# Optimization experiments

Measured on AMD Instinct MI355X. Metric: run time of the kernel, lower is better.

Reference implementation:

```python
import jax, jax.numpy as jnp
import numpy as np

WIN_SIZE = 11
SIGMA = 1.5
DATA_RANGE = 1.0
K1, K2 = 0.01, 0.03


def _gaussian_1d(size=WIN_SIZE, sigma=SIGMA):
    coords = np.arange(size, dtype=np.float32) - (size - 1) / 2.0
    g = np.exp(-(coords ** 2) / (2.0 * sigma ** 2))
    g = g / g.sum()
    return jnp.asarray(g, dtype=jnp.float32)


def _gaussian_blur(x):
    # Separable depthwise Gaussian blur, VALID padding (matches pytorch-msssim).
    B, C, H, W = x.shape
    g = _gaussian_1d().astype(x.dtype)
    kh = jnp.tile(g.reshape(1, 1, WIN_SIZE, 1), (C, 1, 1, 1))
    kw = jnp.tile(g.reshape(1, 1, 1, WIN_SIZE), (C, 1, 1, 1))
    dn = ('NCHW', 'OIHW', 'NCHW')
    x = jax.lax.conv_general_dilated(x, kh, (1, 1), 'VALID',
                                     dimension_numbers=dn, feature_group_count=C)
    x = jax.lax.conv_general_dilated(x, kw, (1, 1), 'VALID',
                                     dimension_numbers=dn, feature_group_count=C)
    return x


def _ssim(X, Y):
    C1 = (K1 * DATA_RANGE) ** 2
    C2 = (K2 * DATA_RANGE) ** 2

    mu1 = _gaussian_blur(X)
    mu2 = _gaussian_blur(Y)
    mu1_sq = mu1 * mu1
    mu2_sq = mu2 * mu2
    mu1_mu2 = mu1 * mu2

    sigma1_sq = _gaussian_blur(X * X) - mu1_sq
    sigma2_sq = _gaussian_blur(Y * Y) - mu2_sq
    sigma12 = _gaussian_blur(X * Y) - mu1_mu2

    cs_map = (2.0 * sigma12 + C2) / (sigma1_sq + sigma2_sq + C2)
    ssim_map = ((2.0 * mu1_mu2 + C1) / (mu1_sq + mu2_sq + C1)) * cs_map

    ssim_per_channel = ssim_map.mean(axis=(2, 3))  # [B, C]
    return ssim_per_channel


def setup_inputs() -> dict:
    key = jax.random.key(0)
    k1, k2 = jax.random.split(key)
    predictions = jax.random.uniform(k1, (32, 3, 512, 512), dtype=jnp.float32)
    labels = jax.random.uniform(k2, (32, 3, 512, 512), dtype=jnp.float32)
    return {"predictions": predictions, "labels": labels}


def reference(predictions, labels):
    ssim_per_channel = _ssim(predictions, labels)
    # nonnegative_ssim=True -> relu; size_average=True -> scalar mean
    ssim_val = jax.nn.relu(ssim_per_channel).mean()
    return 1.0 - ssim_val
```

## Files before the change

kernel.cpp:

```cpp
#include <hip/hip_runtime.h>


#define IMG 512
#define OUT_DIM 502
#define WIN 11
#define BH 32
#define NPHASE (BH + WIN - 1)
#define NPLANES 96

#define GAUSS_INIT {0.00102838f, 0.00759875f, 0.03600077f, 0.10936071f, \
                    0.21300553f, 0.26601172f, 0.21300553f, 0.10936071f, \
                    0.03600077f, 0.00759875f, 0.00102838f}

template<int PH>
__device__ __forceinline__ void phase_step(
    int base, int r0, int c, int cbase,
    const float* __restrict__ Xp, const float* __restrict__ Yp,
    float w0, float w1, float w2, float w3, float w4, float w5,
    float w6, float w7, float w8, float w9, float w10, float w11,
    float (&a)[5][WIN], float& local) {
    constexpr float G[WIN] = GAUSS_INIT;
    const int p = base + PH;
    if (p >= NPHASE) return;
    const int rr = min(r0 + p, IMG - 1);
    const float* px = Xp + rr * IMG + cbase;
    const float* py = Yp + rr * IMG + cbase;

    float h0 = 0.f, h1 = 0.f, h2 = 0.f, h3 = 0.f, h4 = 0.f;
#define PAIR(i, ka, kb) do {                                      \
        const float2 xv = *(const float2*)(px + 2 * (i));         \
        const float2 yv = *(const float2*)(py + 2 * (i));         \
        h0 = fmaf(w##ka, xv.x, h0);                               \
        h1 = fmaf(w##ka, yv.x, h1);                               \
        h2 = fmaf(w##ka, xv.x * xv.x, h2);                        \
        h3 = fmaf(w##ka, yv.x * yv.x, h3);                        \
        h4 = fmaf(w##ka, xv.x * yv.x, h4);                        \
        h0 = fmaf(w##kb, xv.y, h0);                               \
        h1 = fmaf(w##kb, yv.y, h1);                               \
        h2 = fmaf(w##kb, xv.y * xv.y, h2);                        \
        h3 = fmaf(w##kb, yv.y * yv.y, h3);                        \
        h4 = fmaf(w##kb, xv.y * yv.y, h4);                        \
    } while (0)
    PAIR(0, 0, 1); PAIR(1, 2, 3); PAIR(2, 4, 5);
    PAIR(3, 6, 7); PAIR(4, 8, 9); PAIR(5, 10, 11);
#undef PAIR

#define ACC(d) do {                                               \
        constexpr int s = (PH - (d) + 2 * WIN) % WIN;             \
        constexpr float g = G[(d)];                               \
        if ((d) == 0) {                                           \
            a[0][s] = g * h0; a[1][s] = g * h1; a[2][s] = g * h2; \
            a[3][s] = g * h3; a[4][s] = g * h4;                   \
        } else {                                                  \
            a[0][s] = fmaf(g, h0, a[0][s]);                       \
            a[1][s] = fmaf(g, h1, a[1][s]);                       \
            a[2][s] = fmaf(g, h2, a[2][s]);                       \
            a[3][s] = fmaf(g, h3, a[3][s]);                       \
            a[4][s] = fmaf(g, h4, a[4][s]);                       \
        }                                                         \
    } while (0)
    ACC(0); ACC(1); ACC(2); ACC(3); ACC(4); ACC(5);
    ACC(6); ACC(7); ACC(8); ACC(9); ACC(10);
#undef ACC

    if (p >= WIN - 1) {
        const int o = r0 + p - (WIN - 1);
        if (o < OUT_DIM && c < OUT_DIM) {
            constexpr int se = (PH + 1) % WIN;
            const float C1 = 0.0001f, C2 = 0.0009f;
            const float m1 = a[0][se], m2 = a[1][se];
            const float m1sq = m1 * m1, m2sq = m2 * m2, m12 = m1 * m2;
            const float s1  = a[2][se] - m1sq;
            const float s2  = a[3][se] - m2sq;
            const float s12 = a[4][se] - m12;
            const float num = (2.f * m12 + C1) * (2.f * s12 + C2);
            const float den = (m1sq + m2sq + C1) * (s1 + s2 + C2);
            local += num * __builtin_amdgcn_rcpf(den);
        }
    }
}

__global__ __launch_bounds__(256)
__attribute__((amdgpu_waves_per_eu(2, 4)))
void ssim_stream(const float* __restrict__ X,
                 const float* __restrict__ Y,
                 float* __restrict__ planeSums) {
    constexpr float G[WIN] = GAUSS_INIT;
    const int tid = threadIdx.x;
    const int r0 = blockIdx.x * BH;
    const int c = (blockIdx.y << 8) + tid;
    const int plane = blockIdx.z;
    const size_t pbase = (size_t)plane * IMG * IMG;
    const float* Xp = X + pbase;
    const float* Yp = Y + pbase;
    const int cbase = min(c & ~1, IMG - 12);

    const bool odd = (c & 1) != 0;
    const float w0  = odd ? 0.f   : G[0];
    const float w1  = odd ? G[0]  : G[1];
    const float w2  = odd ? G[1]  : G[2];
    const float w3  = odd ? G[2]  : G[3];
    const float w4  = odd ? G[3]  : G[4];
    const float w5  = odd ? G[4]  : G[5];
    const float w6  = odd ? G[5]  : G[6];
    const float w7  = odd ? G[6]  : G[7];
    const float w8  = odd ? G[7]  : G[8];
    const float w9  = odd ? G[8]  : G[9];
    const float w10 = odd ? G[9]  : G[10];
    const float w11 = odd ? G[10] : 0.f;

    float a[5][WIN];
    float local = 0.f;

    for (int base = 0; base < 44; base += WIN) {
        phase_step<0>(base, r0, c, cbase, Xp, Yp, w0,w1,w2,w3,w4,w5,w6,w7,w8,w9,w10,w11, a, local);
        phase_step<1>(base, r0, c, cbase, Xp, Yp, w0,w1,w2,w3,w4,w5,w6,w7,w8,w9,w10,w11, a, local);
        phase_step<2>(base, r0, c, cbase, Xp, Yp, w0,w1,w2,w3,w4,w5,w6,w7,w8,w9,w10,w11, a, local);
        phase_step<3>(base, r0, c, cbase, Xp, Yp, w0,w1,w2,w3,w4,w5,w6,w7,w8,w9,w10,w11, a, local);
        phase_step<4>(base, r0, c, cbase, Xp, Yp, w0,w1,w2,w3,w4,w5,w6,w7,w8,w9,w10,w11, a, local);
        phase_step<5>(base, r0, c, cbase, Xp, Yp, w0,w1,w2,w3,w4,w5,w6,w7,w8,w9,w10,w11, a, local);
        phase_step<6>(base, r0, c, cbase, Xp, Yp, w0,w1,w2,w3,w4,w5,w6,w7,w8,w9,w10,w11, a, local);
        phase_step<7>(base, r0, c, cbase, Xp, Yp, w0,w1,w2,w3,w4,w5,w6,w7,w8,w9,w10,w11, a, local);
        phase_step<8>(base, r0, c, cbase, Xp, Yp, w0,w1,w2,w3,w4,w5,w6,w7,w8,w9,w10,w11, a, local);
        phase_step<9>(base, r0, c, cbase, Xp, Yp, w0,w1,w2,w3,w4,w5,w6,w7,w8,w9,w10,w11, a, local);
        phase_step<10>(base, r0, c, cbase, Xp, Yp, w0,w1,w2,w3,w4,w5,w6,w7,w8,w9,w10,w11, a, local);
    }

    #pragma unroll
    for (int off = 32; off > 0; off >>= 1)
        local += __shfl_down(local, off, 64);
    __shared__ float red[4];
    if ((tid & 63) == 0) red[tid >> 6] = local;
    __syncthreads();
    if (tid == 0)
        atomicAdd(&planeSums[plane], (red[0] + red[1]) + (red[2] + red[3]));
}

__global__ __launch_bounds__(128) void ssim_finalize(const float* __restrict__ planeSums,
                                                     float* __restrict__ out) {
    const int tid = threadIdx.x;
    float v = 0.f;
    if (tid < NPLANES) {
        const float m = planeSums[tid] * (1.0f / (float)(OUT_DIM * OUT_DIM));
        v = fmaxf(m, 0.f);
    }
    #pragma unroll
    for (int off = 32; off > 0; off >>= 1)
        v += __shfl_down(v, off, 64);
    __shared__ float red[2];
    if ((tid & 63) == 0) red[tid >> 6] = v;
    __syncthreads();
    if (tid == 0) out[0] = 1.0f - (red[0] + red[1]) * (1.0f / (float)NPLANES);
}

extern "C" void kernel_launch(void* const* d_in, const int* in_sizes, int n_in,
                              void* d_out, int out_size, void* d_ws, size_t ws_size,
                              hipStream_t stream) {
    const float* X = (const float*)d_in[0];
    const float* Y = (const float*)d_in[1];
    float* out = (float*)d_out;
    float* ws  = (float*)d_ws;

    hipMemsetAsync(ws, 0, NPLANES * sizeof(float), stream);

    dim3 grid((OUT_DIM + BH - 1) / BH, 2, NPLANES);
    ssim_stream<<<grid, 256, 0, stream>>>(X, Y, ws);
    ssim_finalize<<<1, 128, 0, stream>>>(ws, out);
}
```

Baseline: 331.8 us.

## Compute two adjacent output columns per thread to share loads and products

Each thread now produces two adjacent output columns instead of one. The x*x, y*y and x*y products and the row loads are computed once and feed both horizontal filters, replacing the per-thread odd/even weight selection. The grid's column dimension is removed, so the launch uses half as many threads. In exchange, each thread carries twice as many vertical accumulators (110 floats), which raises register pressure and may lower occupancy or cause spills.

```diff
diff --git a/kernel.cpp b/kernel.cpp
--- a/kernel.cpp
+++ b/kernel.cpp
@@ -14,49 +14,70 @@
 
 template<int PH>
 __device__ __forceinline__ void phase_step(
-    int base, int r0, int c, int cbase,
+    int base, int r0row, int c0, int cbase,
     const float* __restrict__ Xp, const float* __restrict__ Yp,
-    float w0, float w1, float w2, float w3, float w4, float w5,
-    float w6, float w7, float w8, float w9, float w10, float w11,
-    float (&a)[5][WIN], float& local) {
+    float (&a)[5][2][WIN], float& local) {
     constexpr float G[WIN] = GAUSS_INIT;
     const int p = base + PH;
     if (p >= NPHASE) return;
-    const int rr = min(r0 + p, IMG - 1);
+    const int rr = min(r0row + p, IMG - 1);
     const float* px = Xp + rr * IMG + cbase;
     const float* py = Yp + rr * IMG + cbase;
 
-    float h0 = 0.f, h1 = 0.f, h2 = 0.f, h3 = 0.f, h4 = 0.f;
-#define PAIR(i, ka, kb) do {                                      \
+    float h0a = 0.f, h1a = 0.f, h2a = 0.f, h3a = 0.f, h4a = 0.f;
+    float h0b = 0.f, h1b = 0.f, h2b = 0.f, h3b = 0.f, h4b = 0.f;
+#define ELT(j, xe, ye) do {                                       \
+        const float xx = (xe) * (xe);                             \
+        const float yy = (ye) * (ye);                             \
+        const float xy = (xe) * (ye);                             \
+        if ((j) <= 10) {                                          \
+            const float ga = G[(j) <= 10 ? (j) : 0];              \
+            h0a = fmaf(ga, (xe), h0a);                            \
+            h1a = fmaf(ga, (ye), h1a);                            \
+            h2a = fmaf(ga, xx, h2a);                              \
+            h3a = fmaf(ga, yy, h3a);                              \
+            h4a = fmaf(ga, xy, h4a);                              \
+        }                                                         \
+        if ((j) >= 1) {                                           \
+            const float gb = G[(j) >= 1 ? (j) - 1 : 0];           \
+            h0b = fmaf(gb, (xe), h0b);                            \
+            h1b = fmaf(gb, (ye), h1b);                            \
+            h2b = fmaf(gb, xx, h2b);                              \
+            h3b = fmaf(gb, yy, h3b);                              \
+            h4b = fmaf(gb, xy, h4b);                              \
+        }                                                         \
+    } while (0)
+#define PAIR(i) do {                                              \
         const float2 xv = *(const float2*)(px + 2 * (i));         \
         const float2 yv = *(const float2*)(py + 2 * (i));         \
-        h0 = fmaf(w##ka, xv.x, h0);                               \
-        h1 = fmaf(w##ka, yv.x, h1);                               \
-        h2 = fmaf(w##ka, xv.x * xv.x, h2);                        \
-        h3 = fmaf(w##ka, yv.x * yv.x, h3);                        \
-        h4 = fmaf(w##ka, xv.x * yv.x, h4);                        \
-        h0 = fmaf(w##kb, xv.y, h0);                               \
-        h1 = fmaf(w##kb, yv.y, h1);                               \
-        h2 = fmaf(w##kb, xv.y * xv.y, h2);                        \
-        h3 = fmaf(w##kb, yv.y * yv.y, h3);                        \
-        h4 = fmaf(w##kb, xv.y * yv.y, h4);                        \
+        ELT(2 * (i),     xv.x, yv.x);                             \
+        ELT(2 * (i) + 1, xv.y, yv.y);                             \
     } while (0)
-    PAIR(0, 0, 1); PAIR(1, 2, 3); PAIR(2, 4, 5);
-    PAIR(3, 6, 7); PAIR(4, 8, 9); PAIR(5, 10, 11);
+    PAIR(0); PAIR(1); PAIR(2); PAIR(3); PAIR(4); PAIR(5);
 #undef PAIR
+#undef ELT
 
 #define ACC(d) do {                                               \
-        constexpr int s = (PH - (d) + 2 * WIN) % WIN;             \
-        constexpr float g = G[(d)];                               \
+        const int s = (PH - (d) + 2 * WIN) % WIN;                 \
+        const float g = G[(d)];                                   \
         if ((d) == 0) {                                           \
-            a[0][s] = g * h0; a[1][s] = g * h1; a[2][s] = g * h2; \
-            a[3][s] = g * h3; a[4][s] = g * h4;                   \
+            a[0][0][s] = g * h0a; a[1][0][s] = g * h1a;           \
+            a[2][0][s] = g * h2a; a[3][0][s] = g * h3a;           \
+            a[4][0][s] = g * h4a;                                 \
+            a[0][1][s] = g * h0b; a[1][1][s] = g * h1b;           \
+            a[2][1][s] = g * h2b; a[3][1][s] = g * h3b;           \
+            a[4][1][s] = g * h4b;                                 \
         } else {                                                  \
-            a[0][s] = fmaf(g, h0, a[0][s]);                       \
-            a[1][s] = fmaf(g, h1, a[1][s]);                       \
-            a[2][s] = fmaf(g, h2, a[2][s]);                       \
-            a[3][s] = fmaf(g, h3, a[3][s]);                       \
-            a[4][s] = fmaf(g, h4, a[4][s]);                       \
+            a[0][0][s] = fmaf(g, h0a, a[0][0][s]);                \
+            a[1][0][s] = fmaf(g, h1a, a[1][0][s]);                \
+            a[2][0][s] = fmaf(g, h2a, a[2][0][s]);                \
+            a[3][0][s] = fmaf(g, h3a, a[3][0][s]);                \
+            a[4][0][s] = fmaf(g, h4a, a[4][0][s]);                \
+            a[0][1][s] = fmaf(g, h0b, a[0][1][s]);                \
+            a[1][1][s] = fmaf(g, h1b, a[1][1][s]);                \
+            a[2][1][s] = fmaf(g, h2b, a[2][1][s]);                \
+            a[3][1][s] = fmaf(g, h3b, a[3][1][s]);                \
+            a[4][1][s] = fmaf(g, h4b, a[4][1][s]);                \
         }                                                         \
     } while (0)
     ACC(0); ACC(1); ACC(2); ACC(3); ACC(4); ACC(5);
@@ -64,18 +85,21 @@
 #undef ACC
 
     if (p >= WIN - 1) {
-        const int o = r0 + p - (WIN - 1);
-        if (o < OUT_DIM && c < OUT_DIM) {
-            constexpr int se = (PH + 1) % WIN;
+        const int o = r0row + p - (WIN - 1);
+        if (o < OUT_DIM && c0 < OUT_DIM) {
+            const int se = (PH + 1) % WIN;
             const float C1 = 0.0001f, C2 = 0.0009f;
-            const float m1 = a[0][se], m2 = a[1][se];
-            const float m1sq = m1 * m1, m2sq = m2 * m2, m12 = m1 * m2;
-            const float s1  = a[2][se] - m1sq;
-            const float s2  = a[3][se] - m2sq;
-            const float s12 = a[4][se] - m12;
-            const float num = (2.f * m12 + C1) * (2.f * s12 + C2);
-            const float den = (m1sq + m2sq + C1) * (s1 + s2 + C2);
-            local += num * __builtin_amdgcn_rcpf(den);
+            #pragma unroll
+            for (int cc = 0; cc < 2; ++cc) {
+                const float m1 = a[0][cc][se], m2 = a[1][cc][se];
+                const float m1sq = m1 * m1, m2sq = m2 * m2, m12 = m1 * m2;
+                const float s1  = a[2][cc][se] - m1sq;
+                const float s2  = a[3][cc][se] - m2sq;
+                const float s12 = a[4][cc][se] - m12;
+                const float num = (2.f * m12 + C1) * (2.f * s12 + C2);
+                const float den = (m1sq + m2sq + C1) * (s1 + s2 + C2);
+                local += num * __builtin_amdgcn_rcpf(den);
+            }
         }
     }
 }
@@ -85,45 +109,30 @@
 void ssim_stream(const float* __restrict__ X,
                  const float* __restrict__ Y,
                  float* __restrict__ planeSums) {
-    constexpr float G[WIN] = GAUSS_INIT;
     const int tid = threadIdx.x;
-    const int r0 = blockIdx.x * BH;
-    const int c = (blockIdx.y << 8) + tid;
-    const int plane = blockIdx.z;
+    const int r0row = blockIdx.x * BH;
+    const int plane = blockIdx.y;
     const size_t pbase = (size_t)plane * IMG * IMG;
     const float* Xp = X + pbase;
     const float* Yp = Y + pbase;
-    const int cbase = min(c & ~1, IMG - 12);
+    const int c0 = tid << 1;
+    const int cbase = min(c0, IMG - 12);
 
-    const bool odd = (c & 1) != 0;
-    const float w0  = odd ? 0.f   : G[0];
-    const float w1  = odd ? G[0]  : G[1];
-    const float w2  = odd ? G[1]  : G[2];
-    const float w3  = odd ? G[2]  : G[3];
-    const float w4  = odd ? G[3]  : G[4];
-    const float w5  = odd ? G[4]  : G[5];
-    const float w6  = odd ? G[5]  : G[6];
-    const float w7  = odd ? G[6]  : G[7];
-    const float w8  = odd ? G[7]  : G[8];
-    const float w9  = odd ? G[8]  : G[9];
-    const float w10 = odd ? G[9]  : G[10];
-    const float w11 = odd ? G[10] : 0.f;
-
-    float a[5][WIN];
+    float a[5][2][WIN];
     float local = 0.f;
 
     for (int base = 0; base < 44; base += WIN) {
-        phase_step<0>(base, r0, c, cbase, Xp, Yp, w0,w1,w2,w3,w4,w5,w6,w7,w8,w9,w10,w11, a, local);
-        phase_step<1>(base, r0, c, cbase, Xp, Yp, w0,w1,w2,w3,w4,w5,w6,w7,w8,w9,w10,w11, a, local);
-        phase_step<2>(base, r0, c, cbase, Xp, Yp, w0,w1,w2,w3,w4,w5,w6,w7,w8,w9,w10,w11, a, local);
-        phase_step<3>(base, r0, c, cbase, Xp, Yp, w0,w1,w2,w3,w4,w5,w6,w7,w8,w9,w10,w11, a, local);
-        phase_step<4>(base, r0, c, cbase, Xp, Yp, w0,w1,w2,w3,w4,w5,w6,w7,w8,w9,w10,w11, a, local);
-        phase_step<5>(base, r0, c, cbase, Xp, Yp, w0,w1,w2,w3,w4,w5,w6,w7,w8,w9,w10,w11, a, local);
-        phase_step<6>(base, r0, c, cbase, Xp, Yp, w0,w1,w2,w3,w4,w5,w6,w7,w8,w9,w10,w11, a, local);
-        phase_step<7>(base, r0, c, cbase, Xp, Yp, w0,w1,w2,w3,w4,w5,w6,w7,w8,w9,w10,w11, a, local);
-        phase_step<8>(base, r0, c, cbase, Xp, Yp, w0,w1,w2,w3,w4,w5,w6,w7,w8,w9,w10,w11, a, local);
-        phase_step<9>(base, r0, c, cbase, Xp, Yp, w0,w1,w2,w3,w4,w5,w6,w7,w8,w9,w10,w11, a, local);
-        phase_step<10>(base, r0, c, cbase, Xp, Yp, w0,w1,w2,w3,w4,w5,w6,w7,w8,w9,w10,w11, a, local);
+        phase_step<0>(base, r0row, c0, cbase, Xp, Yp, a, local);
+        phase_step<1>(base, r0row, c0, cbase, Xp, Yp, a, local);
+        phase_step<2>(base, r0row, c0, cbase, Xp, Yp, a, local);
+        phase_step<3>(base, r0row, c0, cbase, Xp, Yp, a, local);
+        phase_step<4>(base, r0row, c0, cbase, Xp, Yp, a, local);
+        phase_step<5>(base, r0row, c0, cbase, Xp, Yp, a, local);
+        phase_step<6>(base, r0row, c0, cbase, Xp, Yp, a, local);
+        phase_step<7>(base, r0row, c0, cbase, Xp, Yp, a, local);
+        phase_step<8>(base, r0row, c0, cbase, Xp, Yp, a, local);
+        phase_step<9>(base, r0row, c0, cbase, Xp, Yp, a, local);
+        phase_step<10>(base, r0row, c0, cbase, Xp, Yp, a, local);
     }
 
     #pragma unroll
@@ -163,7 +172,7 @@
 
     hipMemsetAsync(ws, 0, NPLANES * sizeof(float), stream);
 
-    dim3 grid((OUT_DIM + BH - 1) / BH, 2, NPLANES);
+    dim3 grid((OUT_DIM + BH - 1) / BH, NPLANES);
     ssim_stream<<<grid, 256, 0, stream>>>(X, Y, ws);
     ssim_finalize<<<1, 128, 0, stream>>>(ws, out);
 }
```

Result: slower. 361.0 us (+8.8%).
